# Kernel tuning notes

Hardware: AMD Instinct MI355X
Metric: run time of the kernel (lower is better)

## Reference

```python
import jax, jax.numpy as jnp
import numpy as np

N = 50000
E = 500000
IN_DIM = 384
HID = 128
HEADS = 4
OUT_DIM = 384
NEG_SLOPE = 0.2


def gat_conv(x, edge_index, W, att_src, att_dst, bias):
    """PyG GATConv (concat=True, add_self_loops=True, eval mode).
    x: [N, F_in]; edge_index: [2, E] (row 0 = source j, row 1 = target i);
    W: [F_in, H*C]; att_src/att_dst: [H, C]; bias: [H*C].
    """
    n = x.shape[0]
    # add self loops
    loops = jnp.arange(n, dtype=edge_index.dtype)
    src = jnp.concatenate([edge_index[0], loops])
    dst = jnp.concatenate([edge_index[1], loops])

    h = (x @ W).reshape(n, HEADS, -1)              # [N, H, C]
    a_src = jnp.einsum('nhc,hc->nh', h, att_src)   # [N, H]
    a_dst = jnp.einsum('nhc,hc->nh', h, att_dst)   # [N, H]

    e = a_src[src] + a_dst[dst]                    # [E', H]
    e = jax.nn.leaky_relu(e, NEG_SLOPE)
    # segment softmax over incoming edges of each target node
    e_max = jax.ops.segment_max(e, dst, num_segments=n)
    e_exp = jnp.exp(e - e_max[dst])
    denom = jax.ops.segment_sum(e_exp, dst, num_segments=n)
    alpha = e_exp / denom[dst]                     # [E', H]

    msg = h[src] * alpha[:, :, None]               # [E', H, C]
    out = jax.ops.segment_sum(msg, dst, num_segments=n)  # [N, H, C]
    return out.reshape(n, -1) + bias


def setup_inputs() -> dict:
    key = jax.random.key(0)
    ks = jax.random.split(key, 12)
    s_in = 1.0 / np.sqrt(IN_DIM)
    s_h = 1.0 / np.sqrt(HEADS * HID)
    return {
        'x': jax.random.normal(ks[0], (N, IN_DIM), dtype=jnp.float32),
        'edge_index': jax.random.randint(ks[1], (2, E), 0, N, dtype=jnp.int32),
        'W1': jax.random.normal(ks[2], (IN_DIM, HEADS * HID), dtype=jnp.float32) * s_in,
        'a1_src': jax.random.normal(ks[3], (HEADS, HID), dtype=jnp.float32) * s_in,
        'a1_dst': jax.random.normal(ks[4], (HEADS, HID), dtype=jnp.float32) * s_in,
        'b1': jnp.zeros((HEADS * HID,), dtype=jnp.float32),
        'W2': jax.random.normal(ks[5], (HEADS * HID, HEADS * HID), dtype=jnp.float32) * s_h,
        'a2_src': jax.random.normal(ks[6], (HEADS, HID), dtype=jnp.float32) * s_h,
        'a2_dst': jax.random.normal(ks[7], (HEADS, HID), dtype=jnp.float32) * s_h,
        'b2': jnp.zeros((HEADS * HID,), dtype=jnp.float32),
        'Wfc': jax.random.normal(ks[8], (HEADS * HID, OUT_DIM), dtype=jnp.float32) * s_h,
        'bfc': jnp.zeros((OUT_DIM,), dtype=jnp.float32),
    }


def reference(x, edge_index, W1, a1_src, a1_dst, b1, W2, a2_src, a2_dst, b2, Wfc, bfc):
    h = jax.nn.relu(gat_conv(x, edge_index, W1, a1_src, a1_dst, b1))
    h = jax.nn.relu(gat_conv(h, edge_index, W2, a2_src, a2_dst, b2))
    return h @ Wfc + bfc  # [N, OUT_DIM]
```

## Files before the change

kernel.cpp:

```cpp
#include <hip/hip_runtime.h>
#include <cfloat>
#include <cstdint>

#define HEADS 4
#define HIDC 128
#define HC 512
#define NEG 0.2f

typedef _Float16 half8 __attribute__((ext_vector_type(8)));
typedef _Float16 half2v __attribute__((ext_vector_type(2)));
typedef float floatx4 __attribute__((ext_vector_type(4)));

__global__ __launch_bounds__(256) void mfma_gemm(
    const _Float16* __restrict__ A,
    const _Float16* __restrict__ Bt,
    _Float16* __restrict__ Ch,
    float* __restrict__ Cf,
    const float* __restrict__ bias,
    const float* __restrict__ atts,
    const float* __restrict__ attd,
    float* __restrict__ a_src,
    float* __restrict__ a_dst,
    int M, int N, int K)
{
    __shared__ __align__(16) _Float16 As[128 * 32];
    __shared__ __align__(16) _Float16 Bs[128 * 32];

    const int tid = threadIdx.x;
    const int w = tid >> 6;
    const int lane = tid & 63;
    const int wr = (w >> 1) * 64;
    const int wc = (w & 1) * 64;

    const int rowBase = blockIdx.y * 128;
    const int colBase = blockIdx.x * 128;

    const int sRow0 = (w * 2 + 0) * 16 + (lane >> 2);
    const int sRow1 = (w * 2 + 1) * 16 + (lane >> 2);
    const int sCol = (lane & 3) * 8;

    const _Float16* gA0 = A + (size_t)(rowBase + sRow0) * K + sCol;
    const _Float16* gA1 = A + (size_t)(rowBase + sRow1) * K + sCol;
    const _Float16* gB0 = Bt + (size_t)(colBase + sRow0) * K + sCol;
    const _Float16* gB1 = Bt + (size_t)(colBase + sRow1) * K + sCol;

    _Float16* lA0 = &As[(w * 2 + 0) * 512];
    _Float16* lA1 = &As[(w * 2 + 1) * 512];
    _Float16* lB0 = &Bs[(w * 2 + 0) * 512];
    _Float16* lB1 = &Bs[(w * 2 + 1) * 512];

    floatx4 acc[4][4];
#pragma unroll
    for (int i = 0; i < 4; i++)
#pragma unroll
        for (int j = 0; j < 4; j++) acc[i][j] = {0.f, 0.f, 0.f, 0.f};

    const int q = lane >> 4;
    const int l16 = lane & 15;

    for (int k0 = 0; k0 < K; k0 += 32) {
        __builtin_amdgcn_global_load_lds(
            (const __attribute__((address_space(1))) unsigned int*)(gA0 + k0),
            (__attribute__((address_space(3))) unsigned int*)lA0, 16, 0, 0);
        __builtin_amdgcn_global_load_lds(
            (const __attribute__((address_space(1))) unsigned int*)(gA1 + k0),
            (__attribute__((address_space(3))) unsigned int*)lA1, 16, 0, 0);
        __builtin_amdgcn_global_load_lds(
            (const __attribute__((address_space(1))) unsigned int*)(gB0 + k0),
            (__attribute__((address_space(3))) unsigned int*)lB0, 16, 0, 0);
        __builtin_amdgcn_global_load_lds(
            (const __attribute__((address_space(1))) unsigned int*)(gB1 + k0),
            (__attribute__((address_space(3))) unsigned int*)lB1, 16, 0, 0);
        __syncthreads();

        half8 af[4], bf[4];
#pragma unroll
        for (int i = 0; i < 4; i++)
            af[i] = *(const half8*)&As[(wr + i * 16 + l16) * 32 + q * 8];
#pragma unroll
        for (int j = 0; j < 4; j++)
            bf[j] = *(const half8*)&Bs[(wc + j * 16 + l16) * 32 + q * 8];
#pragma unroll
        for (int i = 0; i < 4; i++)
#pragma unroll
            for (int j = 0; j < 4; j++)
                acc[i][j] = __builtin_amdgcn_mfma_f32_16x16x32_f16(af[i], bf[j], acc[i][j], 0, 0, 0);
        __syncthreads();
    }

    if (Ch) {
#pragma unroll
        for (int i = 0; i < 4; i++)
#pragma unroll
            for (int j = 0; j < 4; j++) {
                const int col = colBase + wc + j * 16 + l16;
#pragma unroll
                for (int r = 0; r < 4; r++) {
                    const int row = rowBase + wr + i * 16 + q * 4 + r;
                    if (row < M) Ch[(size_t)row * N + col] = (_Float16)acc[i][j][r];
                }
            }
    }
    if (Cf) {
#pragma unroll
        for (int i = 0; i < 4; i++)
#pragma unroll
            for (int j = 0; j < 4; j++) {
                const int col = colBase + wc + j * 16 + l16;
                const float bb = bias ? bias[col] : 0.f;
#pragma unroll
                for (int r = 0; r < 4; r++) {
                    const int row = rowBase + wr + i * 16 + q * 4 + r;
                    if (row < M) Cf[(size_t)row * N + col] = acc[i][j][r] + bb;
                }
            }
    }

    if (atts) {
        float* ps = (float*)As;
        float* pd = ps + 256;
        const int head = blockIdx.x;
        float as[4], ad[4];
#pragma unroll
        for (int j = 0; j < 4; j++) {
            const int cl = wc + j * 16 + l16;
            as[j] = atts[head * HIDC + cl];
            ad[j] = attd[head * HIDC + cl];
        }
#pragma unroll
        for (int i = 0; i < 4; i++) {
#pragma unroll
            for (int r = 0; r < 4; r++) {
                float s_ = acc[i][0][r] * as[0] + acc[i][1][r] * as[1]
                         + acc[i][2][r] * as[2] + acc[i][3][r] * as[3];
                float d_ = acc[i][0][r] * ad[0] + acc[i][1][r] * ad[1]
                         + acc[i][2][r] * ad[2] + acc[i][3][r] * ad[3];
#pragma unroll
                for (int mk = 1; mk <= 8; mk <<= 1) {
                    s_ += __shfl_xor(s_, mk);
                    d_ += __shfl_xor(d_, mk);
                }
                if (l16 == 0) {
                    const int rloc = wr + i * 16 + q * 4 + r;
                    ps[(wc >> 6) * 128 + rloc] = s_;
                    pd[(wc >> 6) * 128 + rloc] = d_;
                }
            }
        }
        __syncthreads();
        if (tid < 128) {
            const int row = rowBase + tid;
            if (row < M) {
                a_src[(size_t)row * 4 + head] = ps[tid] + ps[128 + tid];
                a_dst[(size_t)row * 4 + head] = pd[tid] + pd[128 + tid];
            }
        }
    }
}

__global__ void convert_x_kernel(const float* __restrict__ x, _Float16* __restrict__ o, size_t nquads)
{
    size_t i = (size_t)blockIdx.x * blockDim.x + threadIdx.x;
    if (i < nquads) {
        float4 v = *(const float4*)(x + i * 4);
        _Float16* p = o + i * 4;
        p[0] = (_Float16)v.x; p[1] = (_Float16)v.y;
        p[2] = (_Float16)v.z; p[3] = (_Float16)v.w;
    }
}

__global__ void convert_wT_kernel(const float* __restrict__ W, _Float16* __restrict__ Wt, int K, int N)
{
    int k = blockIdx.x * 64 + (threadIdx.x & 63);
    int n = blockIdx.y * 4 + (threadIdx.x >> 6);
    if (k < K && n < N) Wt[(size_t)n * K + k] = (_Float16)W[(size_t)k * N + n];
}

__global__ void count_kernel(const int* __restrict__ dst, int* __restrict__ deg, int E)
{
    int e = blockIdx.x * blockDim.x + threadIdx.x;
    if (e < E) atomicAdd(&deg[dst[e]], 1);
}

__global__ __launch_bounds__(256) void block_sum_kernel(
    const int* __restrict__ deg, int* __restrict__ bsum, int Nn)
{
    int gid = blockIdx.x * 256 + threadIdx.x;
    int v = (gid < Nn) ? deg[gid] : 0;
#pragma unroll
    for (int o = 32; o >= 1; o >>= 1) v += __shfl_xor(v, o);
    __shared__ int ws[4];
    if ((threadIdx.x & 63) == 0) ws[threadIdx.x >> 6] = v;
    __syncthreads();
    if (threadIdx.x == 0) bsum[blockIdx.x] = ws[0] + ws[1] + ws[2] + ws[3];
}

__global__ __launch_bounds__(256) void scan_bsum_kernel(
    const int* __restrict__ bsum, int* __restrict__ bbase, int nb)
{
    __shared__ int s[256];
    const int tid = threadIdx.x;
    int v = (tid < nb) ? bsum[tid] : 0;
    s[tid] = v;
    __syncthreads();
    for (int off = 1; off < 256; off <<= 1) {
        int t = (tid >= off) ? s[tid - off] : 0;
        __syncthreads();
        s[tid] += t;
        __syncthreads();
    }
    if (tid < nb) bbase[tid] = s[tid] - v;
}

__global__ __launch_bounds__(256) void fill_rowptr_kernel(
    const int* __restrict__ deg, const int* __restrict__ bbase,
    int* __restrict__ rowptr, int* __restrict__ cursor, int Nn, int E)
{
    __shared__ int s[256];
    const int tid = threadIdx.x;
    const int gid = blockIdx.x * 256 + tid;
    int v = (gid < Nn) ? deg[gid] : 0;
    s[tid] = v;
    __syncthreads();
    for (int off = 1; off < 256; off <<= 1) {
        int t = (tid >= off) ? s[tid - off] : 0;
        __syncthreads();
        s[tid] += t;
        __syncthreads();
    }
    if (gid < Nn) {
        int r = bbase[blockIdx.x] + s[tid] - v;
        rowptr[gid] = r;
        cursor[gid] = r;
    }
    if (gid == 0) rowptr[Nn] = E;
}

__global__ void fill_kernel(const int* __restrict__ src, const int* __restrict__ dst,
                            int* __restrict__ cursor, int* __restrict__ eidx, int E)
{
    int e = blockIdx.x * blockDim.x + threadIdx.x;
    if (e < E) {
        int d = dst[e];
        int pos = atomicAdd(&cursor[d], 1);
        eidx[pos] = src[e];
    }
}

__global__ __launch_bounds__(256) void gather_kernel(
    const _Float16* __restrict__ h, const float* __restrict__ a_src, const float* __restrict__ a_dst,
    const int* __restrict__ rowptr, const int* __restrict__ eidx,
    const float* __restrict__ bias, _Float16* __restrict__ out)
{
    const int node = blockIdx.x;
    const int tid = threadIdx.x;
    const int wv = tid >> 6;
    const int lane = tid & 63;

    __shared__ __align__(16) float wgt[256][4];
    __shared__ int sidx[256];
    __shared__ float accs[4][HC];
    __shared__ float part[4][4];

    const int beg = rowptr[node];
    const int total = rowptr[node + 1] - beg + 1;
    const float4 ad4 = *(const float4*)(a_dst + (size_t)node * 4);

    float acc[8];
#pragma unroll
    for (int i = 0; i < 8; i++) acc[i] = 0.f;
    float4 dsum = make_float4(0.f, 0.f, 0.f, 0.f);

    const int hd = lane >> 4;
    const _Float16* hrow_base = h + (size_t)lane * 8;

    for (int off = 0; off < total; off += 256) {
        const int clen = min(total - off, 256);
        if (tid < clen) {
            const int e = off + tid;
            const int s = (e == total - 1) ? node : eidx[beg + e];
            sidx[tid] = s;
            float4 as4 = *(const float4*)(a_src + (size_t)s * 4);
            float l0 = as4.x + ad4.x; l0 = l0 > 0.f ? l0 : NEG * l0;
            float l1 = as4.y + ad4.y; l1 = l1 > 0.f ? l1 : NEG * l1;
            float l2 = as4.z + ad4.z; l2 = l2 > 0.f ? l2 : NEG * l2;
            float l3 = as4.w + ad4.w; l3 = l3 > 0.f ? l3 : NEG * l3;
            float4 w4 = make_float4(__expf(l0), __expf(l1), __expf(l2), __expf(l3));
            *(float4*)&wgt[tid][0] = w4;
            dsum.x += w4.x; dsum.y += w4.y; dsum.z += w4.z; dsum.w += w4.w;
        }
        __syncthreads();
        for (int e = wv; e < clen; e += 4) {
            const float w = wgt[e][hd];
            const int s = sidx[e];
            half8 hv = *(const half8*)(hrow_base + (size_t)s * HC);
#pragma unroll
            for (int i = 0; i < 8; i++) acc[i] += w * (float)hv[i];
        }
        __syncthreads();
    }

#pragma unroll
    for (int o = 32; o >= 1; o >>= 1) {
        dsum.x += __shfl_xor(dsum.x, o);
        dsum.y += __shfl_xor(dsum.y, o);
        dsum.z += __shfl_xor(dsum.z, o);
        dsum.w += __shfl_xor(dsum.w, o);
    }
    if (lane == 0) {
        part[wv][0] = dsum.x; part[wv][1] = dsum.y;
        part[wv][2] = dsum.z; part[wv][3] = dsum.w;
    }
    float* ap = &accs[wv][lane * 8];
#pragma unroll
    for (int i = 0; i < 8; i++) ap[i] = acc[i];
    __syncthreads();

    const int ch = tid * 2;
    const int head = tid >> 6;
    const float is = 1.f / (part[0][head] + part[1][head] + part[2][head] + part[3][head]);
    float t0 = accs[0][ch] + accs[1][ch] + accs[2][ch] + accs[3][ch];
    float t1 = accs[0][ch + 1] + accs[1][ch + 1] + accs[2][ch + 1] + accs[3][ch + 1];
    float2 bv = *(const float2*)(bias + ch);
    float o0 = t0 * is + bv.x; o0 = o0 > 0.f ? o0 : 0.f;
    float o1 = t1 * is + bv.y; o1 = o1 > 0.f ? o1 : 0.f;
    half2v ov; ov.x = (_Float16)o0; ov.y = (_Float16)o1;
    *(half2v*)(out + (size_t)node * HC + ch) = ov;
}

extern "C" void kernel_launch(void* const* d_in, const int* in_sizes, int n_in,
                              void* d_out, int out_size, void* d_ws, size_t ws_size,
                              hipStream_t stream)
{
    const float* x   = (const float*)d_in[0];
    const int*   ei  = (const int*)d_in[1];
    const float* W1  = (const float*)d_in[2];
    const float* a1s = (const float*)d_in[3];
    const float* a1d = (const float*)d_in[4];
    const float* b1  = (const float*)d_in[5];
    const float* W2  = (const float*)d_in[6];
    const float* a2s = (const float*)d_in[7];
    const float* a2d = (const float*)d_in[8];
    const float* b2  = (const float*)d_in[9];
    const float* Wfc = (const float*)d_in[10];
    const float* bfc = (const float*)d_in[11];
    float* out = (float*)d_out;

    const int Nn  = in_sizes[0] / 384;
    const int E   = in_sizes[1] / 2;
    const int IN  = 384;
    const int OUT = in_sizes[11];
    const int Mp  = ((Nn + 127) / 128) * 128;
    const int nb  = (Nn + 255) / 256;

    uint8_t* p = (uint8_t*)d_ws;
    auto alloc = [&](size_t bytes) {
        uint8_t* r = p;
        p += (bytes + 255) & ~(size_t)255;
        return r;
    };
    _Float16* Ah_x = (_Float16*)alloc((size_t)Mp * IN * 2);
    _Float16* Ah_g = (_Float16*)alloc((size_t)Mp * HC * 2);
    _Float16* Hh   = (_Float16*)alloc((size_t)Mp * HC * 2);
    _Float16* Wt1  = (_Float16*)alloc((size_t)HC * IN * 2);
    _Float16* Wt2  = (_Float16*)alloc((size_t)HC * HC * 2);
    _Float16* Wt3  = (_Float16*)alloc((size_t)OUT * HC * 2);
    float* a_src   = (float*)alloc((size_t)Nn * 4 * 4);
    float* a_dst   = (float*)alloc((size_t)Nn * 4 * 4);
    int* deg       = (int*)alloc((size_t)Nn * 4);
    int* rowptr    = (int*)alloc((size_t)(Nn + 1) * 4);
    int* cursor    = (int*)alloc((size_t)Nn * 4);
    int* eidx      = (int*)alloc((size_t)E * 4);
    int* bsum      = (int*)alloc((size_t)nb * 4);
    int* bbase     = (int*)alloc((size_t)nb * 4);

    const int* e_src = ei;
    const int* e_dst = ei + E;

    {
        size_t nq = (size_t)Nn * IN / 4;
        convert_x_kernel<<<(nq + 255) / 256, 256, 0, stream>>>(x, Ah_x, nq);
        dim3 gw1((IN + 63) / 64, HC / 4);
        convert_wT_kernel<<<gw1, 256, 0, stream>>>(W1, Wt1, IN, HC);
        dim3 gw2((HC + 63) / 64, HC / 4);
        convert_wT_kernel<<<gw2, 256, 0, stream>>>(W2, Wt2, HC, HC);
        dim3 gw3((HC + 63) / 64, OUT / 4);
        convert_wT_kernel<<<gw3, 256, 0, stream>>>(Wfc, Wt3, HC, OUT);
    }

    hipMemsetAsync(deg, 0, Nn * sizeof(int), stream);
    const int eb = (E + 255) / 256;
    count_kernel<<<eb, 256, 0, stream>>>(e_dst, deg, E);
    block_sum_kernel<<<nb, 256, 0, stream>>>(deg, bsum, Nn);
    scan_bsum_kernel<<<1, 256, 0, stream>>>(bsum, bbase, nb);
    fill_rowptr_kernel<<<nb, 256, 0, stream>>>(deg, bbase, rowptr, cursor, Nn, E);
    fill_kernel<<<eb, 256, 0, stream>>>(e_src, e_dst, cursor, eidx, E);

    const dim3 gg1(HC / 128, Mp / 128);

    mfma_gemm<<<gg1, 256, 0, stream>>>(Ah_x, Wt1, Hh, nullptr, nullptr,
                                       a1s, a1d, a_src, a_dst, Nn, HC, IN);
    gather_kernel<<<Nn, 256, 0, stream>>>(Hh, a_src, a_dst, rowptr, eidx, b1, Ah_g);

    mfma_gemm<<<gg1, 256, 0, stream>>>(Ah_g, Wt2, Hh, nullptr, nullptr,
                                       a2s, a2d, a_src, a_dst, Nn, HC, HC);
    gather_kernel<<<Nn, 256, 0, stream>>>(Hh, a_src, a_dst, rowptr, eidx, b2, Ah_g);

    const dim3 gg3(OUT / 128, Mp / 128);
    mfma_gemm<<<gg3, 256, 0, stream>>>(Ah_g, Wt3, nullptr, out, bfc,
                                       nullptr, nullptr, nullptr, nullptr, Nn, OUT, HC);
}
```

Baseline: 603.0 us.

## Precompute per-edge attention weights in a separate kernel and unroll gather loop

Adds a destination array to the CSR fill and a new edge_weight_kernel that computes the exponentiated leaky-relu attention weights for all edges in one coalesced, edge-parallel pass. The gather kernel then loads precomputed float4 weights instead of doing a dependent random a_src lookup plus exp per edge. It also unrolls the feature-accumulation loop by two to keep more row loads in flight. This costs an extra kernel launch per layer and 16 bytes per edge of weight traffic written and read back, plus an extra edst write.

```diff
diff --git a/kernel.cpp b/kernel.cpp
--- a/kernel.cpp
+++ b/kernel.cpp
@@ -237,19 +237,42 @@
 }
 
 __global__ void fill_kernel(const int* __restrict__ src, const int* __restrict__ dst,
-                            int* __restrict__ cursor, int* __restrict__ eidx, int E)
+                            int* __restrict__ cursor, int* __restrict__ eidx,
+                            int* __restrict__ edst, int E)
 {
     int e = blockIdx.x * blockDim.x + threadIdx.x;
     if (e < E) {
         int d = dst[e];
         int pos = atomicAdd(&cursor[d], 1);
         eidx[pos] = src[e];
+        edst[pos] = d;
+    }
+}
+
+__global__ __launch_bounds__(256) void edge_weight_kernel(
+    const int* __restrict__ eidx, const int* __restrict__ edst,
+    const float* __restrict__ a_src, const float* __restrict__ a_dst,
+    float4* __restrict__ wedge, int E)
+{
+    int p = blockIdx.x * 256 + threadIdx.x;
+    if (p < E) {
+        int s = eidx[p];
+        int d = edst[p];
+        float4 as4 = *(const float4*)(a_src + (size_t)s * 4);
+        float4 ad4 = *(const float4*)(a_dst + (size_t)d * 4);
+        float l0 = as4.x + ad4.x; l0 = l0 > 0.f ? l0 : NEG * l0;
+        float l1 = as4.y + ad4.y; l1 = l1 > 0.f ? l1 : NEG * l1;
+        float l2 = as4.z + ad4.z; l2 = l2 > 0.f ? l2 : NEG * l2;
+        float l3 = as4.w + ad4.w; l3 = l3 > 0.f ? l3 : NEG * l3;
+        wedge[p] = make_float4(__expf(l0), __expf(l1), __expf(l2), __expf(l3));
     }
 }
 
 __global__ __launch_bounds__(256) void gather_kernel(
-    const _Float16* __restrict__ h, const float* __restrict__ a_src, const float* __restrict__ a_dst,
+    const _Float16* __restrict__ h, const float* __restrict__ a_src,
+    const float* __restrict__ a_dst,
     const int* __restrict__ rowptr, const int* __restrict__ eidx,
+    const float4* __restrict__ wedge,
     const float* __restrict__ bias, _Float16* __restrict__ out)
 {
     const int node = blockIdx.x;
@@ -257,14 +280,14 @@
     const int wv = tid >> 6;
     const int lane = tid & 63;
 
-    __shared__ __align__(16) float wgt[256][4];
+    __shared__ __align__(16) float4 wgt[256];
     __shared__ int sidx[256];
     __shared__ float accs[4][HC];
     __shared__ float part[4][4];
 
     const int beg = rowptr[node];
-    const int total = rowptr[node + 1] - beg + 1;
-    const float4 ad4 = *(const float4*)(a_dst + (size_t)node * 4);
+    const int nE = rowptr[node + 1] - beg;
+    const int total = nE + 1;
 
     float acc[8];
 #pragma unroll
@@ -278,24 +301,45 @@
         const int clen = min(total - off, 256);
         if (tid < clen) {
             const int e = off + tid;
-            const int s = (e == total - 1) ? node : eidx[beg + e];
+            float4 w4;
+            int s;
+            if (e == nE) {
+                s = node;
+                float4 as4 = *(const float4*)(a_src + (size_t)node * 4);
+                float4 ad4 = *(const float4*)(a_dst + (size_t)node * 4);
+                float l0 = as4.x + ad4.x; l0 = l0 > 0.f ? l0 : NEG * l0;
+                float l1 = as4.y + ad4.y; l1 = l1 > 0.f ? l1 : NEG * l1;
+                float l2 = as4.z + ad4.z; l2 = l2 > 0.f ? l2 : NEG * l2;
+                float l3 = as4.w + ad4.w; l3 = l3 > 0.f ? l3 : NEG * l3;
+                w4 = make_float4(__expf(l0), __expf(l1), __expf(l2), __expf(l3));
+            } else {
+                s = eidx[beg + e];
+                w4 = wedge[beg + e];
+            }
             sidx[tid] = s;
-            float4 as4 = *(const float4*)(a_src + (size_t)s * 4);
-            float l0 = as4.x + ad4.x; l0 = l0 > 0.f ? l0 : NEG * l0;
-            float l1 = as4.y + ad4.y; l1 = l1 > 0.f ? l1 : NEG * l1;
-            float l2 = as4.z + ad4.z; l2 = l2 > 0.f ? l2 : NEG * l2;
-            float l3 = as4.w + ad4.w; l3 = l3 > 0.f ? l3 : NEG * l3;
-            float4 w4 = make_float4(__expf(l0), __expf(l1), __expf(l2), __expf(l3));
-            *(float4*)&wgt[tid][0] = w4;
+            wgt[tid] = w4;
             dsum.x += w4.x; dsum.y += w4.y; dsum.z += w4.z; dsum.w += w4.w;
         }
         __syncthreads();
-        for (int e = wv; e < clen; e += 4) {
-            const float w = wgt[e][hd];
-            const int s = sidx[e];
-            half8 hv = *(const half8*)(hrow_base + (size_t)s * HC);
-#pragma unroll
-            for (int i = 0; i < 8; i++) acc[i] += w * (float)hv[i];
+        int e = wv;
+        for (; e + 4 < clen; e += 8) {
+            const int s0 = sidx[e];
+            const int s1 = sidx[e + 4];
+            const float w0 = ((const float*)&wgt[e])[hd];
+            const float w1 = ((const float*)&wgt[e + 4])[hd];
+            half8 hv0 = *(const half8*)(hrow_base + (size_t)s0 * HC);
+            half8 hv1 = *(const half8*)(hrow_base + (size_t)s1 * HC);
+#pragma unroll
+            for (int i = 0; i < 8; i++) acc[i] += w0 * (float)hv0[i];
+#pragma unroll
+            for (int i = 0; i < 8; i++) acc[i] += w1 * (float)hv1[i];
+        }
+        if (e < clen) {
+            const int s0 = sidx[e];
+            const float w0 = ((const float*)&wgt[e])[hd];
+            half8 hv0 = *(const half8*)(hrow_base + (size_t)s0 * HC);
+#pragma unroll
+            for (int i = 0; i < 8; i++) acc[i] += w0 * (float)hv0[i];
         }
         __syncthreads();
     }
@@ -371,6 +415,8 @@
     int* rowptr    = (int*)alloc((size_t)(Nn + 1) * 4);
     int* cursor    = (int*)alloc((size_t)Nn * 4);
     int* eidx      = (int*)alloc((size_t)E * 4);
+    int* edst      = (int*)alloc((size_t)E * 4);
+    float4* wedge  = (float4*)alloc((size_t)E * 16);
     int* bsum      = (int*)alloc((size_t)nb * 4);
     int* bbase     = (int*)alloc((size_t)nb * 4);
 
@@ -394,17 +440,19 @@
     block_sum_kernel<<<nb, 256, 0, stream>>>(deg, bsum, Nn);
     scan_bsum_kernel<<<1, 256, 0, stream>>>(bsum, bbase, nb);
     fill_rowptr_kernel<<<nb, 256, 0, stream>>>(deg, bbase, rowptr, cursor, Nn, E);
-    fill_kernel<<<eb, 256, 0, stream>>>(e_src, e_dst, cursor, eidx, E);
+    fill_kernel<<<eb, 256, 0, stream>>>(e_src, e_dst, cursor, eidx, edst, E);
 
     const dim3 gg1(HC / 128, Mp / 128);
 
     mfma_gemm<<<gg1, 256, 0, stream>>>(Ah_x, Wt1, Hh, nullptr, nullptr,
                                        a1s, a1d, a_src, a_dst, Nn, HC, IN);
-    gather_kernel<<<Nn, 256, 0, stream>>>(Hh, a_src, a_dst, rowptr, eidx, b1, Ah_g);
+    edge_weight_kernel<<<eb, 256, 0, stream>>>(eidx, edst, a_src, a_dst, wedge, E);
+    gather_kernel<<<Nn, 256, 0, stream>>>(Hh, a_src, a_dst, rowptr, eidx, wedge, b1, Ah_g);
 
     mfma_gemm<<<gg1, 256, 0, stream>>>(Ah_g, Wt2, Hh, nullptr, nullptr,
                                        a2s, a2d, a_src, a_dst, Nn, HC, HC);
-    gather_kernel<<<Nn, 256, 0, stream>>>(Hh, a_src, a_dst, rowptr, eidx, b2, Ah_g);
+    edge_weight_kernel<<<eb, 256, 0, stream>>>(eidx, edst, a_src, a_dst, wedge, E);
+    gather_kernel<<<Nn, 256, 0, stream>>>(Hh, a_src, a_dst, rowptr, eidx, wedge, b2, Ah_g);
 
     const dim3 gg3(OUT / 128, Mp / 128);
     mfma_gemm<<<gg3, 256, 0, stream>>>(Ah_g, Wt3, nullptr, out, bfc,
```

After: 596.3 us. About the same (-1.1%).
